# Kernel optimization log

Measured on AMD Instinct MI355X. Metric: run time of the kernel, lower is better.

The kernel has to match this reference:

```python
import jax, jax.numpy as jnp
import numpy as np

N_NODES = 500_000
HIDDEN = 128
REDUCED = HIDDEN // 2
N_GRAPHS = 4096


def setup_inputs() -> dict:
    key = jax.random.key(0)
    k_x, k_b, k_w1, k_w2 = jax.random.split(key, 4)
    x = jax.random.normal(k_x, (N_NODES, HIDDEN), dtype=jnp.float32)
    batch = jnp.sort(jax.random.randint(k_b, (N_NODES,), 0, N_GRAPHS, dtype=jnp.int64))
    # Xavier-uniform init like the torch module; biases zero.
    lim1 = float(np.sqrt(6.0 / (HIDDEN + REDUCED)))
    lim2 = float(np.sqrt(6.0 / (REDUCED + HIDDEN)))
    W1 = jax.random.uniform(k_w1, (HIDDEN, REDUCED), minval=-lim1, maxval=lim1, dtype=jnp.float32)
    b1 = jnp.zeros((REDUCED,), dtype=jnp.float32)
    W2 = jax.random.uniform(k_w2, (REDUCED, HIDDEN), minval=-lim2, maxval=lim2, dtype=jnp.float32)
    b2 = jnp.zeros((HIDDEN,), dtype=jnp.float32)
    return {"x": x, "batch": batch, "size": N_GRAPHS, "W1": W1, "b1": b1, "W2": W2, "b2": b2}


def reference(x, batch, size, W1, b1, W2, b2):
    # scatter-sum pool over graphs: [G, H]
    pooled = jax.ops.segment_sum(x, batch, num_segments=size)
    # squeeze-excite MLP + sigmoid gate
    h = jax.nn.relu(pooled @ W1 + b1)          # [G, H/2]
    y = jax.nn.sigmoid(h @ W2 + b2)            # [G, H]
    # gather-broadcast gate back to nodes and modulate features
    return x * y[batch]                        # [N, H]
```

## Files before the change

### kernel.cpp

```cpp
#include <hip/hip_runtime.h>

#define HIDDEN  128
#define REDUCED 64
#define NGRAPHS 4096

__global__ void pool_kernel(const float* __restrict__ x,
                            const int* __restrict__ batch,
                            float* __restrict__ pooled, int n_nodes) {
    const int g = blockIdx.x;
    const int t = threadIdx.x;
    __shared__ int s_range[2];
    if (t < 2) {
        int lo = 0, hi = n_nodes;
        if (t == 0) {
            while (lo < hi) { int mid = (lo + hi) >> 1; if (batch[mid] <  g) lo = mid + 1; else hi = mid; }
        } else {
            while (lo < hi) { int mid = (lo + hi) >> 1; if (batch[mid] <= g) lo = mid + 1; else hi = mid; }
        }
        s_range[t] = lo;
    }
    __syncthreads();
    const int lo = s_range[0], hi = s_range[1];
    const int r = t >> 5, c = t & 31;

    float4 acc = make_float4(0.f, 0.f, 0.f, 0.f);
    for (int n = lo + r; n < hi; n += 4) {
        const float4 v = ((const float4*)(x + (size_t)n * HIDDEN))[c];
        acc.x += v.x; acc.y += v.y; acc.z += v.z; acc.w += v.w;
    }
    __shared__ float4 red[4][32];
    red[r][c] = acc;
    __syncthreads();
    if (r == 0) {
        const float4 a = red[0][c], b = red[1][c], d = red[2][c], e = red[3][c];
        float4 s;
        s.x = a.x + b.x + d.x + e.x;
        s.y = a.y + b.y + d.y + e.y;
        s.z = a.z + b.z + d.z + e.z;
        s.w = a.w + b.w + d.w + e.w;
        ((float4*)(pooled + (size_t)g * HIDDEN))[c] = s;
    }
}

__global__ void mlp_kernel(const float* __restrict__ pooled,
                           const float* __restrict__ W1, const float* __restrict__ b1,
                           const float* __restrict__ W2, const float* __restrict__ b2,
                           float* __restrict__ y) {
    const int g = blockIdx.x;
    const int t = threadIdx.x;
    __shared__ float p_s[HIDDEN];
    __shared__ float h_s[REDUCED];
    p_s[t] = pooled[(size_t)g * HIDDEN + t];
    __syncthreads();
    if (t < REDUCED) {
        float acc = b1[t];
        #pragma unroll 8
        for (int i = 0; i < HIDDEN; ++i) acc = fmaf(p_s[i], W1[i * REDUCED + t], acc);
        h_s[t] = acc > 0.f ? acc : 0.f;
    }
    __syncthreads();
    float acc = b2[t];
    #pragma unroll 8
    for (int j = 0; j < REDUCED; ++j) acc = fmaf(h_s[j], W2[j * HIDDEN + t], acc);
    y[(size_t)g * HIDDEN + t] = 1.f / (1.f + __expf(-acc));
}

__global__ void modulate_kernel(const float* __restrict__ x,
                                const int* __restrict__ batch,
                                const float* __restrict__ y,
                                float* __restrict__ out, long long total4) {
    const long long idx = (long long)blockIdx.x * blockDim.x + threadIdx.x;
    if (idx >= total4) return;
    const long long n = idx >> 5;
    const int c = (int)(idx & 31);
    const int g = batch[n];
    const float4 xv = ((const float4*)x)[idx];
    const float4 yv = ((const float4*)y)[(size_t)g * (HIDDEN / 4) + c];
    float4 o;
    o.x = xv.x * yv.x; o.y = xv.y * yv.y; o.z = xv.z * yv.z; o.w = xv.w * yv.w;
    ((float4*)out)[idx] = o;
}

extern "C" void kernel_launch(void* const* d_in, const int* in_sizes, int n_in,
                              void* d_out, int out_size, void* d_ws, size_t ws_size,
                              hipStream_t stream) {
    const float* x     = (const float*)d_in[0];
    const int*   batch = (const int*)d_in[1];
    const float* W1 = (const float*)d_in[3];
    const float* b1 = (const float*)d_in[4];
    const float* W2 = (const float*)d_in[5];
    const float* b2 = (const float*)d_in[6];
    float* out = (float*)d_out;

    const int n_nodes = in_sizes[0] / HIDDEN;

    float* pooled = (float*)d_ws;
    float* y      = pooled + (size_t)NGRAPHS * HIDDEN;

    pool_kernel<<<NGRAPHS, 128, 0, stream>>>(x, batch, pooled, n_nodes);
    mlp_kernel<<<NGRAPHS, 128, 0, stream>>>(pooled, W1, b1, W2, b2, y);

    const long long total4 = (long long)n_nodes * (HIDDEN / 4);
    const int blocks = (int)((total4 + 255) / 256);
    modulate_kernel<<<blocks, 256, 0, stream>>>(x, batch, y, out, total4);
}
```

Before: 505.1 us.

## Fuse pooling with gate MLP and use nontemporal loads/stores in modulate

```diff
diff --git a/kernel.cpp b/kernel.cpp
--- a/kernel.cpp
+++ b/kernel.cpp
@@ -4,65 +4,61 @@
 #define REDUCED 64
 #define NGRAPHS 4096
 
-__global__ void pool_kernel(const float* __restrict__ x,
-                            const int* __restrict__ batch,
-                            float* __restrict__ pooled, int n_nodes) {
+typedef float f4 __attribute__((ext_vector_type(4)));
+
+__global__ void pool_mlp_kernel(const float* __restrict__ x,
+                                const int* __restrict__ batch,
+                                const float* __restrict__ W1, const float* __restrict__ b1,
+                                const float* __restrict__ W2, const float* __restrict__ b2,
+                                float* __restrict__ y, int n_nodes) {
     const int g = blockIdx.x;
     const int t = threadIdx.x;
     __shared__ int s_range[2];
-    if (t < 2) {
+    if (t == 0) {
         int lo = 0, hi = n_nodes;
-        if (t == 0) {
-            while (lo < hi) { int mid = (lo + hi) >> 1; if (batch[mid] <  g) lo = mid + 1; else hi = mid; }
-        } else {
-            while (lo < hi) { int mid = (lo + hi) >> 1; if (batch[mid] <= g) lo = mid + 1; else hi = mid; }
-        }
-        s_range[t] = lo;
+        while (lo < hi) { int mid = (lo + hi) >> 1; if (batch[mid] <  g) lo = mid + 1; else hi = mid; }
+        s_range[0] = lo;
+    } else if (t == 64) {
+        int lo = 0, hi = n_nodes;
+        while (lo < hi) { int mid = (lo + hi) >> 1; if (batch[mid] <= g) lo = mid + 1; else hi = mid; }
+        s_range[1] = lo;
     }
     __syncthreads();
     const int lo = s_range[0], hi = s_range[1];
     const int r = t >> 5, c = t & 31;
 
-    float4 acc = make_float4(0.f, 0.f, 0.f, 0.f);
+    f4 acc = {0.f, 0.f, 0.f, 0.f};
     for (int n = lo + r; n < hi; n += 4) {
-        const float4 v = ((const float4*)(x + (size_t)n * HIDDEN))[c];
-        acc.x += v.x; acc.y += v.y; acc.z += v.z; acc.w += v.w;
+        const f4 v = ((const f4*)(x + (size_t)n * HIDDEN))[c];
+        acc += v;
     }
-    __shared__ float4 red[4][32];
+    __shared__ f4 red[4][32];
+    __shared__ float p_s[HIDDEN];
+    __shared__ float h_s[REDUCED];
     red[r][c] = acc;
     __syncthreads();
     if (r == 0) {
-        const float4 a = red[0][c], b = red[1][c], d = red[2][c], e = red[3][c];
-        float4 s;
+        const f4 a = red[0][c], b = red[1][c], d = red[2][c], e = red[3][c];
+        f4 s;
         s.x = a.x + b.x + d.x + e.x;
         s.y = a.y + b.y + d.y + e.y;
         s.z = a.z + b.z + d.z + e.z;
         s.w = a.w + b.w + d.w + e.w;
-        ((float4*)(pooled + (size_t)g * HIDDEN))[c] = s;
-    }
-}
-
-__global__ void mlp_kernel(const float* __restrict__ pooled,
-                           const float* __restrict__ W1, const float* __restrict__ b1,
-                           const float* __restrict__ W2, const float* __restrict__ b2,
-                           float* __restrict__ y) {
-    const int g = blockIdx.x;
-    const int t = threadIdx.x;
-    __shared__ float p_s[HIDDEN];
-    __shared__ float h_s[REDUCED];
-    p_s[t] = pooled[(size_t)g * HIDDEN + t];
-    __syncthreads();
-    if (t < REDUCED) {
-        float acc = b1[t];
-        #pragma unroll 8
-        for (int i = 0; i < HIDDEN; ++i) acc = fmaf(p_s[i], W1[i * REDUCED + t], acc);
-        h_s[t] = acc > 0.f ? acc : 0.f;
+        ((f4*)p_s)[c] = s;
     }
     __syncthreads();
-    float acc = b2[t];
+
+    if (t < REDUCED) {
+        float a1 = b1[t];
+        #pragma unroll 8
+        for (int i = 0; i < HIDDEN; ++i) a1 = fmaf(p_s[i], W1[i * REDUCED + t], a1);
+        h_s[t] = a1 > 0.f ? a1 : 0.f;
+    }
+    __syncthreads();
+    float a2 = b2[t];
     #pragma unroll 8
-    for (int j = 0; j < REDUCED; ++j) acc = fmaf(h_s[j], W2[j * HIDDEN + t], acc);
-    y[(size_t)g * HIDDEN + t] = 1.f / (1.f + __expf(-acc));
+    for (int j = 0; j < REDUCED; ++j) a2 = fmaf(h_s[j], W2[j * HIDDEN + t], a2);
+    y[(size_t)g * HIDDEN + t] = 1.f / (1.f + __expf(-a2));
 }
 
 __global__ void modulate_kernel(const float* __restrict__ x,
@@ -74,11 +70,11 @@
     const long long n = idx >> 5;
     const int c = (int)(idx & 31);
     const int g = batch[n];
-    const float4 xv = ((const float4*)x)[idx];
-    const float4 yv = ((const float4*)y)[(size_t)g * (HIDDEN / 4) + c];
-    float4 o;
+    const f4 xv = __builtin_nontemporal_load((const f4*)x + idx);
+    const f4 yv = ((const f4*)y)[(size_t)g * (HIDDEN / 4) + c];
+    f4 o;
     o.x = xv.x * yv.x; o.y = xv.y * yv.y; o.z = xv.z * yv.z; o.w = xv.w * yv.w;
-    ((float4*)out)[idx] = o;
+    __builtin_nontemporal_store(o, (f4*)out + idx);
 }
 
 extern "C" void kernel_launch(void* const* d_in, const int* in_sizes, int n_in,
@@ -94,11 +90,9 @@
 
     const int n_nodes = in_sizes[0] / HIDDEN;
 
-    float* pooled = (float*)d_ws;
-    float* y      = pooled + (size_t)NGRAPHS * HIDDEN;
+    float* y = (float*)d_ws;
 
-    pool_kernel<<<NGRAPHS, 128, 0, stream>>>(x, batch, pooled, n_nodes);
-    mlp_kernel<<<NGRAPHS, 128, 0, stream>>>(pooled, W1, b1, W2, b2, y);
+    pool_mlp_kernel<<<NGRAPHS, 128, 0, stream>>>(x, batch, W1, b1, W2, b2, y, n_nodes);
 
     const long long total4 = (long long)n_nodes * (HIDDEN / 4);
     const int blocks = (int)((total4 + 255) / 256);
```

After: 485.2 us. -3.9%, faster.
